# Kernel optimization log

Measured on AMD Instinct MI355X. Metric: run time of the kernel, lower is better.

Reference implementation:

```python
import jax, jax.numpy as jnp
import numpy as np

Q_LATTICE = 4      # nested lattice alphabet size
QMAX_ACT = 127.0   # 2**(8-1) - 1 for 8-bit LSQ


def _lattice_quantize(x_blocks, G, Ginv, q):
    # x_blocks: [N, 8] rows are block vectors. Lattice point = z @ G, z integer.
    z = jnp.round(x_blocks @ Ginv)
    half = q // 2
    z_mod = jnp.mod(z + half, q) - half  # nested (mod-q) lattice, centered
    return z_mod @ G


def setup_inputs() -> dict:
    key = jax.random.key(0)
    k1, k2 = jax.random.split(key)
    O, I, BS = 4096, 4096, 8
    rng = np.random.default_rng(0)
    G_np = np.eye(BS, dtype=np.float64) + 0.1 * rng.standard_normal((BS, BS))
    Ginv_np = np.linalg.inv(G_np)
    return {
        "x": jax.random.normal(k1, (256, I), dtype=jnp.float32),
        "weight": jax.random.normal(k2, (O, I), dtype=jnp.float32),
        "bias": jnp.zeros((O,), dtype=jnp.float32),
        "theta_beta": jnp.ones((O, 1), dtype=jnp.float32),
        "alpha": jnp.ones((1,), dtype=jnp.float32),
        "G": jnp.asarray(G_np, dtype=jnp.float32),
        "Ginv": jnp.asarray(Ginv_np, dtype=jnp.float32),
    }


def reference(x, weight, bias, theta_beta, alpha, G, Ginv):
    O, I = weight.shape
    bs = G.shape[0]
    nblk = I // bs
    sg = jax.lax.stop_gradient

    # --- hierarchical nested-lattice weight quantization (row tiling) ---
    W_blocks = weight.reshape(O, nblk, bs)
    # theta_beta [O, k] -> mean over k -> [O, 1, 1], broadcast to all blocks
    scale_w = jnp.mean(theta_beta, axis=-1, keepdims=True)[:, None, :]
    W_scaled = (W_blocks * scale_w).reshape(-1, bs)
    # straight-through lattice quantize
    W_q = W_scaled + sg(_lattice_quantize(W_scaled, G, Ginv, Q_LATTICE) - W_scaled)
    W_q = W_q.reshape(O, I)

    # --- linear ---
    y = x @ W_q.T + bias

    # --- LSQ activation quantization ---
    a = jax.nn.relu(alpha) + 1e-8          # [1]
    y_clipped = y + sg(jnp.clip(y, -a, a) - y)  # ste_clip (clamp detached)
    s = a / QMAX_ACT
    y_scaled = y_clipped / s
    y_round = y_scaled + sg(jnp.round(y_scaled) - y_scaled)  # ste_round
    return y_round * s
```

## Files before the change

### kernel.cpp

```cpp
#include <hip/hip_runtime.h>

typedef __attribute__((ext_vector_type(8))) __bf16 bf16x8;
typedef __attribute__((ext_vector_type(4))) float f32x4;

#define M_ 256
#define N_ 4096
#define K_ 4096
#define SPLITK 4
#define KC (K_ / SPLITK)
#define BM 128
#define BN 64
#define BK 32
#define KSTEPS (KC / BK)
#define NCH 20
#define LDSBUF 20480



__device__ __forceinline__ unsigned short f2bf(float f) {
  unsigned int u = __builtin_bit_cast(unsigned int, f);
  u += 0x7fffu + ((u >> 16) & 1u);
  return (unsigned short)(u >> 16);
}

__device__ __forceinline__ void async16(const void* g, void* l) {
  __builtin_amdgcn_global_load_lds(
      (const __attribute__((address_space(1))) unsigned int*)g,
      (__attribute__((address_space(3))) unsigned int*)l, 16, 0, 0);
}

__device__ __forceinline__ float lsq1(float y, float a, float s) {
  float yc = fminf(fmaxf(y, -a), a);
  return rintf(yc / s) * s;
}


#define NQB ((N_ * K_ / 8) / 256)
#define NXB ((M_ * K_ / 8) / 256)

__global__ __launch_bounds__(256) void k_prep(const float* __restrict__ W,
                                              const float* __restrict__ theta,
                                              const float* __restrict__ Ginv,
                                              const float* __restrict__ x,
                                              const float* __restrict__ G,
                                              unsigned short* __restrict__ zq,
                                              unsigned short* __restrict__ hi,
                                              unsigned short* __restrict__ lo,
                                              int kTheta) {
  __shared__ float Ms[64];
  const int tid = threadIdx.x;
  const bool isQ = blockIdx.x < NQB;
  if (tid < 64) Ms[tid] = isQ ? Ginv[tid] : G[tid];
  __syncthreads();

  if (isQ) {
    const int s = blockIdx.x * 256 + tid;
    const int lane6 = s & 63;
    const int tile = s >> 6;
    const int o  = ((tile >> 7) << 4) + (lane6 & 15);
    const int kb = ((tile & 127) << 2) + (lane6 >> 4);
    const float4* wp = (const float4*)(W + ((size_t)o << 12) + ((size_t)kb << 3));
    const float4 w0 = wp[0], w1 = wp[1];
    float sc = 0.f;
    for (int t = 0; t < kTheta; ++t) sc += theta[o * kTheta + t];
    sc /= (float)kTheta;
    const float wsv[8] = {w0.x * sc, w0.y * sc, w0.z * sc, w0.w * sc,
                          w1.x * sc, w1.y * sc, w1.z * sc, w1.w * sc};
    unsigned int packed[4] = {0u, 0u, 0u, 0u};
    const unsigned long long lut = 0x3F800000BF80C000ull;
#pragma unroll
    for (int i = 0; i < 8; ++i) {
      float t = 0.f;
#pragma unroll
      for (int j = 0; j < 8; ++j)
        t = __fadd_rn(t, __fmul_rn(wsv[j], Ms[j * 8 + i]));
      const int zi = (int)rintf(t);
      const int idx = (zi + 2) & 3;
      const unsigned int h = (unsigned int)((lut >> (idx * 16)) & 0xFFFFull);
      packed[i >> 1] |= h << ((i & 1) * 16);
    }
    *(uint4*)(zq + ((size_t)s << 3)) = make_uint4(packed[0], packed[1], packed[2], packed[3]);
  } else {
    const int s = (blockIdx.x - NQB) * 256 + tid;
    const int lane6 = s & 63;
    const int tile = s >> 6;
    const int m  = ((tile >> 7) << 4) + (lane6 & 15);
    const int kb = ((tile & 127) << 2) + (lane6 >> 4);
    const float4* xp = (const float4*)(x + ((size_t)m << 12) + ((size_t)kb << 3));
    const float4 a0 = xp[0], a1 = xp[1];
    float xv[8] = {a0.x, a0.y, a0.z, a0.w, a1.x, a1.y, a1.z, a1.w};
    unsigned int ph[4] = {0u, 0u, 0u, 0u}, pl[4] = {0u, 0u, 0u, 0u};
#pragma unroll
    for (int i = 0; i < 8; ++i) {
      float t = 0.f;
#pragma unroll
      for (int j = 0; j < 8; ++j) t = fmaf(xv[j], Ms[i * 8 + j], t);
      const unsigned short hb = f2bf(t);
      const float hf = __builtin_bit_cast(float, (unsigned int)hb << 16);
      const unsigned short lb = f2bf(t - hf);
      ph[i >> 1] |= ((unsigned int)hb) << ((i & 1) * 16);
      pl[i >> 1] |= ((unsigned int)lb) << ((i & 1) * 16);
    }
    *(uint4*)(hi + ((size_t)s << 3)) = make_uint4(ph[0], ph[1], ph[2], ph[3]);
    *(uint4*)(lo + ((size_t)s << 3)) = make_uint4(pl[0], pl[1], pl[2], pl[3]);
  }
}


__global__ __launch_bounds__(512, 4) void k_gemm(const unsigned short* __restrict__ xgh,
                                                 const unsigned short* __restrict__ xgl,
                                                 const unsigned short* __restrict__ z,
                                                 float* __restrict__ part) {
  __shared__ uint4 smem4[2 * LDSBUF / 16];
  char* smem = (char*)smem4;

  const int tid = threadIdx.x;
  const int lane = tid & 63, wave = tid >> 6;
  const int wr = wave >> 1, wc = wave & 1;
  const int b = blockIdx.x;
  const int mt = b & 1;
  const int sk = (b >> 1) & 3;
  const int nt = b >> 3;
  const int k0t = sk * (KC / 32);
  const int rowa16 = mt * (BM / 16);
  const int rowb16 = nt * (BN / 16);
  const int lrow = lane & 15, lkg = lane >> 4;

  const unsigned short* src[3];
  unsigned int ldso[3];
#pragma unroll
  for (int ci = 0; ci < 3; ++ci) {
    const int c = ci * 8 + wave;
    if (c < NCH) {
      const unsigned short* P;
      int rt;
      if (c < 8)       { P = xgh; rt = rowa16 + c; }
      else if (c < 16) { P = xgl; rt = rowa16 + (c - 8); }
      else             { P = z;   rt = rowb16 + (c - 16); }
      src[ci] = P + (((size_t)(rt * 128 + k0t)) << 9) + lane * 8;
      ldso[ci] = (unsigned int)c * 1024u;
    } else {
      src[ci] = nullptr;
      ldso[ci] = 0;
    }
  }
  const int nchunk = (wave < 4) ? 3 : 2;

  f32x4 acc[2][2] = {};

  for (int ci = 0; ci < nchunk; ++ci) async16(src[ci], smem + ldso[ci]);
  __syncthreads();

  for (int ks = 0; ks < KSTEPS; ++ks) {
    const int cur = (ks & 1) * LDSBUF;
    const int nxt = LDSBUF - cur;
    if (ks + 1 < KSTEPS) {
      for (int ci = 0; ci < nchunk; ++ci)
        async16(src[ci] + (size_t)(ks + 1) * 512, smem + nxt + ldso[ci]);
    }

    bf16x8 bfr[2], ah[2], al[2];
#pragma unroll
    for (int nf = 0; nf < 2; ++nf)
      bfr[nf] = *(const bf16x8*)(smem + cur + (16 + wc * 2 + nf) * 1024 + lane * 16);
#pragma unroll
    for (int mf = 0; mf < 2; ++mf) {
      ah[mf] = *(const bf16x8*)(smem + cur + (wr * 2 + mf) * 1024 + lane * 16);
      al[mf] = *(const bf16x8*)(smem + cur + (8 + wr * 2 + mf) * 1024 + lane * 16);
    }
#pragma unroll
    for (int mf = 0; mf < 2; ++mf)
#pragma unroll
      for (int nf = 0; nf < 2; ++nf) {
        acc[mf][nf] = __builtin_amdgcn_mfma_f32_16x16x32_bf16(ah[mf], bfr[nf], acc[mf][nf], 0, 0, 0);
        acc[mf][nf] = __builtin_amdgcn_mfma_f32_16x16x32_bf16(al[mf], bfr[nf], acc[mf][nf], 0, 0, 0);
      }
    __syncthreads();
  }

  float* pb = part + (size_t)sk * (M_ * N_);
  const int row_a = mt * BM, row_b = nt * BN;
#pragma unroll
  for (int mf = 0; mf < 2; ++mf)
#pragma unroll
    for (int nf = 0; nf < 2; ++nf)
#pragma unroll
      for (int r = 0; r < 4; ++r) {
        const int m = row_a + wr * 32 + mf * 16 + lkg * 4 + r;
        const int n = row_b + wc * 32 + nf * 16 + lrow;
        pb[(size_t)m * N_ + n] = acc[mf][nf][r];
      }
}


__global__ __launch_bounds__(256) void k_epi(const float* __restrict__ part,
                                             const float* __restrict__ bias,
                                             const float* __restrict__ alpha,
                                             float* __restrict__ out) {
  const int i4 = blockIdx.x * 256 + threadIdx.x;
  const size_t off = (size_t)i4 * 4;
  const float4 p0 = *(const float4*)(part + off);
  const float4 p1 = *(const float4*)(part + (size_t)1 * M_ * N_ + off);
  const float4 p2 = *(const float4*)(part + (size_t)2 * M_ * N_ + off);
  const float4 p3 = *(const float4*)(part + (size_t)3 * M_ * N_ + off);
  const int n = (int)(off & (N_ - 1));
  const float4 bv = *(const float4*)(bias + n);
  const float a = fmaxf(alpha[0], 0.f) + 1e-8f;
  const float s = a / 127.0f;
  float4 o;
  o.x = lsq1(((p0.x + p1.x) + p2.x) + p3.x + bv.x, a, s);
  o.y = lsq1(((p0.y + p1.y) + p2.y) + p3.y + bv.y, a, s);
  o.z = lsq1(((p0.z + p1.z) + p2.z) + p3.z + bv.z, a, s);
  o.w = lsq1(((p0.w + p1.w) + p2.w) + p3.w + bv.w, a, s);
  *(float4*)(out + off) = o;
}


extern "C" void kernel_launch(void* const* d_in, const int* in_sizes, int n_in,
                              void* d_out, int out_size, void* d_ws, size_t ws_size,
                              hipStream_t stream) {
  const float* x     = (const float*)d_in[0];
  const float* W     = (const float*)d_in[1];
  const float* bias  = (const float*)d_in[2];
  const float* theta = (const float*)d_in[3];
  const float* alpha = (const float*)d_in[4];
  const float* G     = (const float*)d_in[5];
  const float* Ginv  = (const float*)d_in[6];
  float* out = (float*)d_out;

  const int O = in_sizes[2];
  const int kTheta = in_sizes[3] / O;

  char* ws = (char*)d_ws;
  unsigned short* zq  = (unsigned short*)ws;
  unsigned short* xgh = (unsigned short*)(ws + 33554432);
  unsigned short* xgl = (unsigned short*)(ws + 35651584);
  float* part = (float*)(ws + 37748736);
  if (ws_size < 54525952) return;

  k_prep<<<NQB + NXB, 256, 0, stream>>>(W, theta, Ginv, x, G, zq, xgh, xgl, kTheta);
  k_gemm<<<2 * 4 * 64, 512, 0, stream>>>(xgh, xgl, zq, part);
  k_epi<<<(M_ * N_ / 4) / 256, 256, 0, stream>>>(part, bias, alpha, out);
}
```

Before: 52.40 us.

## Deepen GEMM async LDS pipeline to four stages with explicit vmcnt waits

Replaces the double-buffered global-to-LDS prefetch in the split-K GEMM with a 4-deep ring buffer. Three k-steps are issued ahead, and each step waits on a per-wave vmcnt threshold plus a raw s_barrier instead of a full __syncthreads. The goal is to hide more global load latency behind MFMA work. LDS use doubles to 80 KB per block, which may lower occupancy from the launch-bound target of 4 blocks. Correctness also depends on the hand-counted vmcnt values matching each wave's chunk count.

```diff
diff --git a/kernel.cpp b/kernel.cpp
--- a/kernel.cpp
+++ b/kernel.cpp
@@ -14,6 +14,7 @@
 #define KSTEPS (KC / BK)
 #define NCH 20
 #define LDSBUF 20480
+#define DEPTH 4
 
 
 
@@ -32,6 +33,12 @@
 __device__ __forceinline__ float lsq1(float y, float a, float s) {
   float yc = fminf(fmaxf(y, -a), a);
   return rintf(yc / s) * s;
+}
+
+template <int VH, int VL>
+__device__ __forceinline__ void waitv(int wave) {
+  if (wave < 4) asm volatile("s_waitcnt vmcnt(%0)" ::"n"(VH) : "memory");
+  else          asm volatile("s_waitcnt vmcnt(%0)" ::"n"(VL) : "memory");
 }
 
 
@@ -111,7 +118,7 @@
                                                  const unsigned short* __restrict__ xgl,
                                                  const unsigned short* __restrict__ z,
                                                  float* __restrict__ part) {
-  __shared__ uint4 smem4[2 * LDSBUF / 16];
+  __shared__ uint4 smem4[DEPTH * LDSBUF / 16];
   char* smem = (char*)smem4;
 
   const int tid = threadIdx.x;
@@ -148,17 +155,13 @@
 
   f32x4 acc[2][2] = {};
 
-  for (int ci = 0; ci < nchunk; ++ci) async16(src[ci], smem + ldso[ci]);
-  __syncthreads();
-
-  for (int ks = 0; ks < KSTEPS; ++ks) {
-    const int cur = (ks & 1) * LDSBUF;
-    const int nxt = LDSBUF - cur;
-    if (ks + 1 < KSTEPS) {
-      for (int ci = 0; ci < nchunk; ++ci)
-        async16(src[ci] + (size_t)(ks + 1) * 512, smem + nxt + ldso[ci]);
-    }
-
+  auto issue = [&](int kb) {
+    const int wo = (kb & (DEPTH - 1)) * LDSBUF;
+    for (int ci = 0; ci < nchunk; ++ci)
+      async16(src[ci] + (size_t)kb * 512, smem + wo + ldso[ci]);
+  };
+  auto compute = [&](int ks) {
+    const int cur = (ks & (DEPTH - 1)) * LDSBUF;
     bf16x8 bfr[2], ah[2], al[2];
 #pragma unroll
     for (int nf = 0; nf < 2; ++nf)
@@ -175,8 +178,22 @@
         acc[mf][nf] = __builtin_amdgcn_mfma_f32_16x16x32_bf16(ah[mf], bfr[nf], acc[mf][nf], 0, 0, 0);
         acc[mf][nf] = __builtin_amdgcn_mfma_f32_16x16x32_bf16(al[mf], bfr[nf], acc[mf][nf], 0, 0, 0);
       }
-    __syncthreads();
+  };
+
+  issue(0); issue(1); issue(2);
+
+  for (int ks = 0; ks < KSTEPS - 2; ++ks) {
+    waitv<6, 4>(wave);
+    __builtin_amdgcn_s_barrier();
+    if (ks + 3 < KSTEPS) issue(ks + 3);
+    compute(ks);
   }
+  waitv<3, 2>(wave);
+  __builtin_amdgcn_s_barrier();
+  compute(KSTEPS - 2);
+  waitv<0, 0>(wave);
+  __builtin_amdgcn_s_barrier();
+  compute(KSTEPS - 1);
 
   float* pb = part + (size_t)sk * (M_ * N_);
   const int row_a = mt * BM, row_b = nt * BN;
@@ -239,6 +256,6 @@
   if (ws_size < 54525952) return;
 
   k_prep<<<NQB + NXB, 256, 0, stream>>>(W, theta, Ginv, x, G, zq, xgh, xgl, kTheta);
-  k_gemm<<<2 * 4 * 64, 512, 0, stream>>>(xgh, xgl, zq, part);
+  k_gemm<<<2 * SPLITK * 64, 512, 0, stream>>>(xgh, xgl, zq, part);
   k_epi<<<(M_ * N_ / 4) / 256, 256, 0, stream>>>(part, bias, alpha, out);
 }
```

Result: no change. 52.01 us (-0.7%).

## Pack lattice codes to 2 bits and decode to bf16 in the GEMM

Applied to the files above, without the earlier changes.

The prep kernel now stores each 8-element weight block as a 16-bit word of 2-bit lattice indices instead of eight bf16 values. The GEMM loads these words through registers, decodes them with a small lookup, and writes bf16 fragments into LDS, replacing async global-to-LDS copies for the B operand. This cuts the intermediate weight buffer by a factor of eight, reducing DRAM write and read traffic. The cost is extra ALU decode work and synchronous register-path loads in half the waves of the GEMM inner loop.

```diff
diff --git a/kernel.cpp b/kernel.cpp
--- a/kernel.cpp
+++ b/kernel.cpp
@@ -34,6 +34,19 @@
   return rintf(yc / s) * s;
 }
 
+#define ZLUT 0x3F800000BF80C000ull
+
+__device__ __forceinline__ uint4 zdec(unsigned int w) {
+  unsigned int d[4];
+#pragma unroll
+  for (int p = 0; p < 4; ++p) {
+    const unsigned int lo = (unsigned int)((ZLUT >> (((w >> (4 * p)) & 3u) * 16)) & 0xFFFFull);
+    const unsigned int hi = (unsigned int)((ZLUT >> (((w >> (4 * p + 2)) & 3u) * 16)) & 0xFFFFull);
+    d[p] = lo | (hi << 16);
+  }
+  return make_uint4(d[0], d[1], d[2], d[3]);
+}
+
 
 #define NQB ((N_ * K_ / 8) / 256)
 #define NXB ((M_ * K_ / 8) / 256)
@@ -43,7 +56,7 @@
                                               const float* __restrict__ Ginv,
                                               const float* __restrict__ x,
                                               const float* __restrict__ G,
-                                              unsigned short* __restrict__ zq,
+                                              unsigned short* __restrict__ z2,
                                               unsigned short* __restrict__ hi,
                                               unsigned short* __restrict__ lo,
                                               int kTheta) {
@@ -54,6 +67,7 @@
   __syncthreads();
 
   if (isQ) {
+#pragma clang fp contract(off)
     const int s = blockIdx.x * 256 + tid;
     const int lane6 = s & 63;
     const int tile = s >> 6;
@@ -66,20 +80,17 @@
     sc /= (float)kTheta;
     const float wsv[8] = {w0.x * sc, w0.y * sc, w0.z * sc, w0.w * sc,
                           w1.x * sc, w1.y * sc, w1.z * sc, w1.w * sc};
-    unsigned int packed[4] = {0u, 0u, 0u, 0u};
-    const unsigned long long lut = 0x3F800000BF80C000ull;
+    unsigned int word = 0u;
 #pragma unroll
     for (int i = 0; i < 8; ++i) {
       float t = 0.f;
 #pragma unroll
       for (int j = 0; j < 8; ++j)
-        t = __fadd_rn(t, __fmul_rn(wsv[j], Ms[j * 8 + i]));
+        t = t + wsv[j] * Ms[j * 8 + i];
       const int zi = (int)rintf(t);
-      const int idx = (zi + 2) & 3;
-      const unsigned int h = (unsigned int)((lut >> (idx * 16)) & 0xFFFFull);
-      packed[i >> 1] |= h << ((i & 1) * 16);
-    }
-    *(uint4*)(zq + ((size_t)s << 3)) = make_uint4(packed[0], packed[1], packed[2], packed[3]);
+      word |= (unsigned int)((zi + 2) & 3) << (2 * i);
+    }
+    z2[s] = (unsigned short)word;
   } else {
     const int s = (blockIdx.x - NQB) * 256 + tid;
     const int lane6 = s & 63;
@@ -109,7 +120,7 @@
 
 __global__ __launch_bounds__(512, 4) void k_gemm(const unsigned short* __restrict__ xgh,
                                                  const unsigned short* __restrict__ xgl,
-                                                 const unsigned short* __restrict__ z,
+                                                 const unsigned short* __restrict__ z2,
                                                  float* __restrict__ part) {
   __shared__ uint4 smem4[2 * LDSBUF / 16];
   char* smem = (char*)smem4;
@@ -126,37 +137,45 @@
   const int rowb16 = nt * (BN / 16);
   const int lrow = lane & 15, lkg = lane >> 4;
 
-  const unsigned short* src[3];
-  unsigned int ldso[3];
-#pragma unroll
-  for (int ci = 0; ci < 3; ++ci) {
-    const int c = ci * 8 + wave;
-    if (c < NCH) {
-      const unsigned short* P;
-      int rt;
-      if (c < 8)       { P = xgh; rt = rowa16 + c; }
-      else if (c < 16) { P = xgl; rt = rowa16 + (c - 8); }
-      else             { P = z;   rt = rowb16 + (c - 16); }
-      src[ci] = P + (((size_t)(rt * 128 + k0t)) << 9) + lane * 8;
-      ldso[ci] = (unsigned int)c * 1024u;
-    } else {
-      src[ci] = nullptr;
-      ldso[ci] = 0;
-    }
-  }
-  const int nchunk = (wave < 4) ? 3 : 2;
+  const unsigned short* asrc[2];
+  int aldo[2];
+#pragma unroll
+  for (int ci = 0; ci < 2; ++ci) {
+    const unsigned short* P = (ci == 0) ? xgh : xgl;
+    asrc[ci] = P + (((size_t)((rowa16 + wave) * 128 + k0t)) << 9) + lane * 8;
+    aldo[ci] = (ci * 8 + wave) * 1024;
+  }
+  const bool brole = (wave < 4);
+  const unsigned short* zsrc = nullptr;
+  int bofs = 0;
+  if (brole) {
+    zsrc = z2 + (((size_t)((rowb16 + wave) * 128 + k0t)) << 6) + lane;
+    bofs = (16 + wave) * 1024 + lane * 16;
+  }
 
   f32x4 acc[2][2] = {};
 
-  for (int ci = 0; ci < nchunk; ++ci) async16(src[ci], smem + ldso[ci]);
+  unsigned int zw = 0;
+#pragma unroll
+  for (int ci = 0; ci < 2; ++ci) async16(asrc[ci], smem + aldo[ci]);
+  if (brole) {
+    zw = zsrc[0];
+    *(uint4*)(smem + bofs) = zdec(zw);
+    zw = zsrc[64];
+  }
   __syncthreads();
 
   for (int ks = 0; ks < KSTEPS; ++ks) {
     const int cur = (ks & 1) * LDSBUF;
     const int nxt = LDSBUF - cur;
     if (ks + 1 < KSTEPS) {
-      for (int ci = 0; ci < nchunk; ++ci)
-        async16(src[ci] + (size_t)(ks + 1) * 512, smem + nxt + ldso[ci]);
+#pragma unroll
+      for (int ci = 0; ci < 2; ++ci)
+        async16(asrc[ci] + (size_t)(ks + 1) * 512, smem + nxt + aldo[ci]);
+      if (brole) {
+        *(uint4*)(smem + nxt + bofs) = zdec(zw);
+        if (ks + 2 < KSTEPS) zw = zsrc[(size_t)(ks + 2) * 64];
+      }
     }
 
     bf16x8 bfr[2], ah[2], al[2];
@@ -232,13 +251,13 @@
   const int kTheta = in_sizes[3] / O;
 
   char* ws = (char*)d_ws;
-  unsigned short* zq  = (unsigned short*)ws;
-  unsigned short* xgh = (unsigned short*)(ws + 33554432);
-  unsigned short* xgl = (unsigned short*)(ws + 35651584);
-  float* part = (float*)(ws + 37748736);
-  if (ws_size < 54525952) return;
-
-  k_prep<<<NQB + NXB, 256, 0, stream>>>(W, theta, Ginv, x, G, zq, xgh, xgl, kTheta);
-  k_gemm<<<2 * 4 * 64, 512, 0, stream>>>(xgh, xgl, zq, part);
+  unsigned short* xgh = (unsigned short*)ws;
+  unsigned short* xgl = (unsigned short*)(ws + 2097152);
+  unsigned short* z2  = (unsigned short*)(ws + 4194304);
+  float* part = (float*)(ws + 8388608);
+  if (ws_size < 25165824) return;
+
+  k_prep<<<NQB + NXB, 256, 0, stream>>>(W, theta, Ginv, x, G, z2, xgh, xgl, kTheta);
+  k_gemm<<<2 * SPLITK * 64, 512, 0, stream>>>(xgh, xgl, z2, part);
   k_epi<<<(M_ * N_ / 4) / 256, 256, 0, stream>>>(part, bias, alpha, out);
 }
```

Result: faster. 49.15 us, median of 2 (-6.2%).
